# Optimization experiments

Measured on AMD Instinct MI355X. Metric: run time of the kernel, lower is better.

## Reference

```python
import jax, jax.numpy as jnp
import numpy as np

B, C, H, W = 8, 384, 32, 32
HEADS = 12


def _relative_position_index(h, w):
    coords_h = np.arange(h)
    coords_w = np.arange(w)
    coords = np.stack(np.meshgrid(coords_h, coords_w, indexing='ij'))  # [2,h,w]
    flat = coords.reshape(2, -1)  # [2, N]
    rel = flat[:, :, None] - flat[:, None, :]  # [2, N, N]
    rel = rel.transpose(1, 2, 0)  # [N, N, 2]
    rel[:, :, 0] += h - 1
    rel[:, :, 1] += w - 1
    rel[:, :, 0] *= 2 * w - 1
    return rel.sum(-1).astype(np.int32)  # [N, N]


def setup_inputs() -> dict:
    key = jax.random.key(0)
    ks = jax.random.split(key, 6)
    std = 0.02
    x = jax.random.normal(ks[0], (B, C, H, W), dtype=jnp.float32)
    q_w = jax.random.normal(ks[1], (C, C), dtype=jnp.float32) * std
    q_b = jnp.zeros((C,), dtype=jnp.float32)
    kv_w = jax.random.normal(ks[2], (2 * C, C), dtype=jnp.float32) * std
    kv_b = jnp.zeros((2 * C,), dtype=jnp.float32)
    proj_w = jax.random.normal(ks[3], (C, C), dtype=jnp.float32) * std
    proj_b = jnp.zeros((C,), dtype=jnp.float32)
    n_table = (2 * H - 1) * (2 * W - 1)
    rpb_table = jax.random.normal(ks[4], (n_table, HEADS), dtype=jnp.float32) * std
    rel_index = jnp.asarray(_relative_position_index(H, W))  # [N, N] int32
    return {"x": x, "q_w": q_w, "q_b": q_b, "kv_w": kv_w, "kv_b": kv_b,
            "proj_w": proj_w, "proj_b": proj_b, "rpb_table": rpb_table,
            "rel_index": rel_index}


def reference(x, q_w, q_b, kv_w, kv_b, proj_w, proj_b, rpb_table, rel_index):
    b, c, h, w = x.shape
    n = h * w
    heads = rpb_table.shape[-1]
    hd = c // heads
    scale = hd ** (-0.5)

    xf = x.reshape(b, c, n)  # 1x1 conv == per-pixel matmul
    q = jnp.einsum('dc,bcn->bdn', q_w, xf) + q_b[:, None]
    q = q.reshape(b, heads, hd, n).transpose(0, 1, 3, 2)  # [b,h,n,hd]
    kv = jnp.einsum('dc,bcn->bdn', kv_w, xf) + kv_b[:, None]
    kv = kv.reshape(b, 2, heads, hd, n)
    k = kv[:, 0].transpose(0, 1, 3, 2)  # [b,h,n,hd]
    v = kv[:, 1].transpose(0, 1, 3, 2)

    attn = jnp.einsum('bhnd,bhmd->bhnm', q, k) * scale  # [b,h,n,n]
    bias = rpb_table[rel_index.reshape(-1)].reshape(n, n, heads)
    bias = bias.transpose(2, 0, 1)  # [h,n,n]
    attn = jax.nn.softmax(attn + bias[None], axis=-1)

    out = jnp.einsum('bhnm,bhmd->bhnd', attn, v)
    out = out.transpose(0, 1, 3, 2).reshape(b, c, h, w)
    out = jnp.einsum('dc,bchw->bdhw', proj_w, out) + proj_b[None, :, None, None]
    return out
```

## Files before the change

kernel.cpp:

```cpp
#include <hip/hip_runtime.h>
#include <hip/hip_bf16.h>

#define B_  8
#define C_  384
#define N_  1024
#define NH_ 12
#define HD_ 32
#define D3_ 1152

typedef __bf16 bf16x8 __attribute__((ext_vector_type(8)));
typedef __bf16 bf16x2 __attribute__((ext_vector_type(2)));
typedef float  f32x4  __attribute__((ext_vector_type(4)));

typedef const __attribute__((address_space(1))) unsigned int guint;
typedef __attribute__((address_space(3))) unsigned int luint;

__device__ __forceinline__ float b2f(ushort u) {
    return __uint_as_float(((unsigned int)u) << 16);
}
__device__ __forceinline__ ushort f2b(float f) {
    unsigned int i = __float_as_uint(f);
    unsigned int r = i + 0x7fffu + ((i >> 16) & 1u);
    return (ushort)(r >> 16);
}
__device__ __forceinline__ unsigned pk2(float a, float b) {
#if __has_builtin(__builtin_amdgcn_cvt_pk_bf16_f32)
    bf16x2 t = __builtin_amdgcn_cvt_pk_bf16_f32(a, b);
    return __builtin_bit_cast(unsigned, t);
#else
    return (unsigned)f2b(a) | ((unsigned)f2b(b) << 16);
#endif
}

#if __has_builtin(__builtin_amdgcn_exp2f)
#define EXP2 __builtin_amdgcn_exp2f
#else
#define EXP2 exp2f
#endif

__device__ __forceinline__ void gl2lds16(const void* g, void* l) {
    __builtin_amdgcn_global_load_lds((guint*)g, (luint*)l, 16, 0, 0);
}

#define C1_ 0.25505654204433796f
#define C2_ 1.4426950408889634f
#define TS_ 3972

__global__ __launch_bounds__(256) void setup(
    const float* __restrict__ x, const float* __restrict__ q_w,
    const float* __restrict__ kv_w, const float* __restrict__ proj_w,
    const float* __restrict__ q_b, const float* __restrict__ kv_b,
    const float* __restrict__ tab,
    ushort* __restrict__ xT, float* __restrict__ tabT,
    ushort* __restrict__ Wall, ushort* __restrict__ PW,
    float* __restrict__ ballf)
{
    __shared__ ushort T[64 * 72];
    const int bx = blockIdx.x, tid = threadIdx.x;

    if (bx < 768) {
        int t = bx;
        int nx = t & 15, cy = (t >> 4) % 6, b = t / 96;
        int n0 = nx * 64, c0 = cy * 64;
        {
            int i = tid >> 2;
            int ns = (tid & 3) * 16;
            const float* src = x + ((size_t)b * C_ + c0 + i) * N_ + n0 + ns;
            #pragma unroll
            for (int k4 = 0; k4 < 4; ++k4) {
                float4 f = *(const float4*)(src + k4 * 4);
                T[(ns + k4 * 4 + 0) * 72 + i] = f2b(f.x);
                T[(ns + k4 * 4 + 1) * 72 + i] = f2b(f.y);
                T[(ns + k4 * 4 + 2) * 72 + i] = f2b(f.z);
                T[(ns + k4 * 4 + 3) * 72 + i] = f2b(f.w);
            }
        }
        __syncthreads();
        {
            int j = tid >> 2;
            int cs = (tid & 3) * 16;
            ushort* dst = xT + ((size_t)b * N_ + n0 + j) * C_ + c0 + cs;
            *(uint4*)dst       = *(const uint4*)&T[j * 72 + cs];
            *(uint4*)(dst + 8) = *(const uint4*)&T[j * 72 + cs + 8];
        }
    } else if (bx < 1346) {
        const int NW4 = 110592, NP4 = 36864, NB4 = 288;
        int t = (bx - 768) * 256 + tid;
        if (t < NW4) {
            int e = t * 4;
            float4 f = (e < 147456) ? *(const float4*)(q_w + e)
                                    : *(const float4*)(kv_w + e - 147456);
            union { uint2 u; ushort s[4]; } o;
            o.u.x = pk2(f.x, f.y); o.u.y = pk2(f.z, f.w);
            *(uint2*)(Wall + e) = o.u;
        } else if (t < NW4 + NP4) {
            int e = (t - NW4) * 4;
            float4 f = *(const float4*)(proj_w + e);
            union { uint2 u; ushort s[4]; } o;
            o.u.x = pk2(f.x, f.y); o.u.y = pk2(f.z, f.w);
            *(uint2*)(PW + e) = o.u;
        } else if (t < NW4 + NP4 + NB4) {
            int e = (t - NW4 - NP4) * 4;
            float4 f = (e < 384) ? *(const float4*)(q_b + e)
                                 : *(const float4*)(kv_b + e - 384);
            *(float4*)(ballf + e) = f;
        }
    } else {
        int h = bx - 1346;
        for (int i = tid; i < 3969; i += 256)
            tabT[h * TS_ + i] = tab[(size_t)(3968 - i) * NH_ + h] * C2_;
        if (tid < 3) tabT[h * TS_ + 3969 + tid] = 0.0f;
    }
}

__global__ __launch_bounds__(256) void qkv_gemm5(
    const ushort* __restrict__ xT, const ushort* __restrict__ Wall,
    const float* __restrict__ ballf, ushort* __restrict__ Qt,
    ushort* __restrict__ Kt, ushort* __restrict__ Vtc)
{
    const int b = blockIdx.z, n0 = blockIdx.x * 128, d0 = blockIdx.y * 128;
    __shared__ ushort As[128 * 32];
    __shared__ ushort Bs[128 * 32];
    const int tid = threadIdx.x;
    const int lane = tid & 63, wave = tid >> 6;
    const int quad = lane >> 4, l16 = lane & 15;
    const int wn = (wave & 1) * 64, wd = (wave >> 1) * 64;

    f32x4 acc[4][4] = {};
    const ushort* xb = xT + ((size_t)b * N_ + n0) * C_;
    const ushort* wb = Wall + (size_t)d0 * C_;
    const int rowA = wave * 16 + (lane >> 2);
    const int fstage = ((lane >> 2) ^ (lane >> 4)) & 3;
    const int coff = ((lane & 3) ^ fstage) * 8;
    const int fread = ((l16 & 3) ^ ((l16 >> 2) & 3));
    const bool isV = (d0 >= 768);

    for (int c0 = 0; c0 < C_; c0 += 32) {
        #pragma unroll
        for (int k = 0; k < 2; ++k) {
            gl2lds16(xb + (size_t)(k * 64 + rowA) * C_ + c0 + coff,
                     &As[(size_t)(k * 256 + wave * 64) * 8]);
            gl2lds16(wb + (size_t)(k * 64 + rowA) * C_ + c0 + coff,
                     &Bs[(size_t)(k * 256 + wave * 64) * 8]);
        }
        __syncthreads();
        bf16x8 af[4], bfr[4];
        #pragma unroll
        for (int i = 0; i < 4; ++i)
            af[i] = *(const bf16x8*)&As[(wn + i * 16 + l16) * 32 + (quad ^ fread) * 8];
        #pragma unroll
        for (int j = 0; j < 4; ++j)
            bfr[j] = *(const bf16x8*)&Bs[(wd + j * 16 + l16) * 32 + (quad ^ fread) * 8];
        if (!isV) {
            #pragma unroll
            for (int i = 0; i < 4; ++i)
                #pragma unroll
                for (int j = 0; j < 4; ++j)
                    acc[i][j] = __builtin_amdgcn_mfma_f32_16x16x32_bf16(bfr[i], af[j], acc[i][j], 0, 0, 0);
        } else {
            #pragma unroll
            for (int i = 0; i < 4; ++i)
                #pragma unroll
                for (int j = 0; j < 4; ++j)
                    acc[i][j] = __builtin_amdgcn_mfma_f32_16x16x32_bf16(af[i], bfr[j], acc[i][j], 0, 0, 0);
        }
        __syncthreads();
    }

    if (!isV) {
        ushort* dst = (d0 < 384) ? Qt : Kt;
        const float sc = (d0 < 384) ? C1_ : 1.0f;
        const int reg0 = (d0 < 384) ? 0 : 384;
        #pragma unroll
        for (int i = 0; i < 4; ++i) {
            int dloc = wd + i * 16;
            int dg = d0 - reg0 + dloc;
            int h = dg >> 5;
            int dc = (dg & 31) + quad * 4;
            float4 bvv = *(const float4*)(ballf + d0 + dloc + quad * 4);
            size_t hb = (size_t)(b * NH_ + h) * N_;
            #pragma unroll
            for (int j = 0; j < 4; ++j) {
                int n = n0 + wn + j * 16 + l16;
                uint2 w;
                w.x = pk2((acc[i][j][0] + bvv.x) * sc, (acc[i][j][1] + bvv.y) * sc);
                w.y = pk2((acc[i][j][2] + bvv.z) * sc, (acc[i][j][3] + bvv.w) * sc);
                *(uint2*)(dst + (hb + n) * 32 + dc) = w;
            }
        }
    } else {
        #pragma unroll
        for (int j = 0; j < 4; ++j) {
            int dloc = wd + j * 16 + l16;
            int vd = d0 - 768 + dloc;
            int h = vd >> 5, dc = vd & 31;
            float bv = ballf[d0 + dloc];
            size_t hbase = (size_t)(b * NH_ + h) * 32768 + dc * 32;
            #pragma unroll
            for (int i = 0; i < 4; ++i) {
                int n = n0 + wn + i * 16 + quad * 4;
                size_t cbase = hbase + (size_t)((n >> 5)) * 1024 + (n & 31);
                uint2 w;
                w.x = pk2(acc[i][j][0] + bv, acc[i][j][1] + bv);
                w.y = pk2(acc[i][j][2] + bv, acc[i][j][3] + bv);
                *(uint2*)(Vtc + cbase) = w;
            }
        }
    }
}

__global__ __launch_bounds__(256) void attn9(
    const ushort* __restrict__ Qt, const ushort* __restrict__ Kt,
    const ushort* __restrict__ Vtc, const float* __restrict__ tabT,
    ushort* __restrict__ O)
{
    const int bid = blockIdx.x;
    const int bh96 = bid % 96;
    const int nx = bid / 96;
    const int b = bh96 / 12, h = bh96 % 12;

    __shared__ float tabL[TS_];
    __shared__ ushort Pa[8192];

    const int tid = threadIdx.x;
    const int lane = tid & 63, wave = tid >> 6;
    const int quad = lane >> 4, l16 = lane & 15;
    const int bh = b * NH_ + h;

    {
        const float* th = tabT + h * TS_;
        int i = tid * 4;
        #pragma unroll
        for (int k = 0; k < 4; ++k) {
            if (i < TS_) *(float4*)&tabL[i] = *(const float4*)&th[i];
            i += 1024;
        }
    }
    __syncthreads();

    const int qs0 = nx * 8 + wave * 2;
    const ushort* Kbh = Kt + (size_t)bh * N_ * 32;
    const ushort* Vbh = Vtc + (size_t)bh * 16 * 2048;

    bf16x8 qf[2];
    #pragma unroll
    for (int st = 0; st < 2; ++st) {
        int q = (qs0 + st) * 16 + l16;
        qf[st] = *(const bf16x8*)(Qt + ((size_t)bh * N_ + q) * 32 + quad * 8);
    }
    int ibx0;
    {
        int q = qs0 * 16 + l16;
        ibx0 = (31 - (q >> 5)) * 63 + (31 - (q & 31));
    }

    bf16x8 ones;
    #pragma unroll
    for (int j = 0; j < 8; ++j) ones[j] = (__bf16)1.0f;

    f32x4 oacc[2][2] = {};
    f32x4 lacc[2] = {};

    ushort* PwBase = &Pa[wave * 2048];
    const int pswz = l16 & 0xE;

    for (int mc = 0; mc < 16; ++mc) {
        const ushort* kp = Kbh + mc * 64 * 32;
        bf16x8 k0 = *(const bf16x8*)(kp + (0 * 16 + l16) * 32 + quad * 8);
        bf16x8 k1 = *(const bf16x8*)(kp + (1 * 16 + l16) * 32 + quad * 8);
        bf16x8 k2 = *(const bf16x8*)(kp + (2 * 16 + l16) * 32 + quad * 8);
        bf16x8 k3 = *(const bf16x8*)(kp + (3 * 16 + l16) * 32 + quad * 8);
        const ushort* vp = Vbh + mc * 2048;
        bf16x8 va[2][2];
        #pragma unroll
        for (int kc = 0; kc < 2; ++kc)
            #pragma unroll
            for (int dt = 0; dt < 2; ++dt)
                va[kc][dt] = *(const bf16x8*)(vp + kc * 1024 + (dt * 16 + l16) * 32 + quad * 8);

        const float* Tb = tabL + ibx0 + mc * 126 + quad * 4;
        f32x4 tvm16, tv0, tv16, tv47, tv63, tv79;
        #pragma unroll
        for (int e = 0; e < 4; ++e) {
            tvm16[e] = Tb[e - 16];
            tv0[e]   = Tb[e];
            tv16[e]  = Tb[e + 16];
            tv47[e]  = Tb[e + 47];
            tv63[e]  = Tb[e + 63];
            tv79[e]  = Tb[e + 79];
        }
        f32x4 cbs[2][4] = {{tv0, tv16, tv63, tv79}, {tvm16, tv0, tv47, tv63}};

        #pragma unroll
        for (int st = 0; st < 2; ++st) {
            f32x4 s0 = __builtin_amdgcn_mfma_f32_16x16x32_bf16(k0, qf[st], cbs[st][0], 0, 0, 0);
            f32x4 s1 = __builtin_amdgcn_mfma_f32_16x16x32_bf16(k1, qf[st], cbs[st][1], 0, 0, 0);
            f32x4 s2 = __builtin_amdgcn_mfma_f32_16x16x32_bf16(k2, qf[st], cbs[st][2], 0, 0, 0);
            f32x4 s3 = __builtin_amdgcn_mfma_f32_16x16x32_bf16(k3, qf[st], cbs[st][3], 0, 0, 0);

            ushort* Pw = PwBase + st * 1024;
            f32x4 sv[4] = {s0, s1, s2, s3};
            #pragma unroll
            for (int t = 0; t < 4; ++t) {
                float p0 = EXP2(sv[t][0]);
                float p1 = EXP2(sv[t][1]);
                float p2 = EXP2(sv[t][2]);
                float p3 = EXP2(sv[t][3]);
                uint2 w;
                w.x = pk2(p0, p1);
                w.y = pk2(p2, p3);
                *(uint2*)(Pw + l16 * 64 + (((t * 4 + quad) ^ pswz) * 4)) = w;
            }
            #pragma unroll
            for (int kc = 0; kc < 2; ++kc) {
                bf16x8 pb = *(const bf16x8*)(Pw + l16 * 64 + (((kc * 8 + quad * 2) ^ pswz) * 4));
                lacc[st]    = __builtin_amdgcn_mfma_f32_16x16x32_bf16(ones, pb, lacc[st], 0, 0, 0);
                oacc[st][0] = __builtin_amdgcn_mfma_f32_16x16x32_bf16(va[kc][0], pb, oacc[st][0], 0, 0, 0);
                oacc[st][1] = __builtin_amdgcn_mfma_f32_16x16x32_bf16(va[kc][1], pb, oacc[st][1], 0, 0, 0);
            }
        }
    }

    #pragma unroll
    for (int st = 0; st < 2; ++st) {
        float inv = 1.0f / lacc[st][0];
        int q = (qs0 + st) * 16 + l16;
        ushort* ob = O + ((size_t)(b * N_ + q)) * C_ + h * HD_;
        #pragma unroll
        for (int dt = 0; dt < 2; ++dt) {
            uint2 w;
            w.x = pk2(oacc[st][dt][0] * inv, oacc[st][dt][1] * inv);
            w.y = pk2(oacc[st][dt][2] * inv, oacc[st][dt][3] * inv);
            *(uint2*)(ob + dt * 16 + quad * 4) = w;
        }
    }
}

__global__ __launch_bounds__(256) void proj_gemm3(
    const ushort* __restrict__ O, const ushort* __restrict__ PW,
    const float* __restrict__ pb, float* __restrict__ out)
{
    const int b = blockIdx.z, n0 = blockIdx.x * 128, d0 = blockIdx.y * 128;
    __shared__ ushort As[128 * 32];
    __shared__ ushort Bs[128 * 32];
    const int tid = threadIdx.x;
    const int lane = tid & 63, wave = tid >> 6;
    const int quad = lane >> 4, l16 = lane & 15;
    const int wa = (wave & 1) * 64, wb = (wave >> 1) * 64;

    f32x4 acc[4][4] = {};
    const ushort* ab = PW + (size_t)d0 * C_;
    const ushort* bbp = O + ((size_t)b * N_ + n0) * C_;
    const int rowA = wave * 16 + (lane >> 2);
    const int fstage = ((lane >> 2) ^ (lane >> 4)) & 3;
    const int coff = ((lane & 3) ^ fstage) * 8;
    const int fread = ((l16 & 3) ^ ((l16 >> 2) & 3));

    for (int c0 = 0; c0 < C_; c0 += 32) {
        #pragma unroll
        for (int k = 0; k < 2; ++k) {
            gl2lds16(ab + (size_t)(k * 64 + rowA) * C_ + c0 + coff,
                     &As[(size_t)(k * 256 + wave * 64) * 8]);
            gl2lds16(bbp + (size_t)(k * 64 + rowA) * C_ + c0 + coff,
                     &Bs[(size_t)(k * 256 + wave * 64) * 8]);
        }
        __syncthreads();
        bf16x8 af[4], bfr[4];
        #pragma unroll
        for (int i = 0; i < 4; ++i)
            af[i] = *(const bf16x8*)&As[(wa + i * 16 + l16) * 32 + (quad ^ fread) * 8];
        #pragma unroll
        for (int j = 0; j < 4; ++j)
            bfr[j] = *(const bf16x8*)&Bs[(wb + j * 16 + l16) * 32 + (quad ^ fread) * 8];
        #pragma unroll
        for (int i = 0; i < 4; ++i)
            #pragma unroll
            for (int j = 0; j < 4; ++j)
                acc[i][j] = __builtin_amdgcn_mfma_f32_16x16x32_bf16(af[i], bfr[j], acc[i][j], 0, 0, 0);
        __syncthreads();
    }

    #pragma unroll
    for (int i = 0; i < 4; ++i) {
        #pragma unroll
        for (int r = 0; r < 4; ++r) {
            int d = d0 + wa + i * 16 + quad * 4 + r;
            float bv = pb[d];
            float* op = out + ((size_t)b * C_ + d) * N_ + n0 + wb;
            #pragma unroll
            for (int j = 0; j < 4; ++j)
                op[j * 16 + l16] = acc[i][j][r] + bv;
        }
    }
}

extern "C" void kernel_launch(void* const* d_in, const int* in_sizes, int n_in,
                              void* d_out, int out_size, void* d_ws, size_t ws_size,
                              hipStream_t stream)
{
    const float* x      = (const float*)d_in[0];
    const float* q_w    = (const float*)d_in[1];
    const float* q_b    = (const float*)d_in[2];
    const float* kv_w   = (const float*)d_in[3];
    const float* kv_b   = (const float*)d_in[4];
    const float* proj_w = (const float*)d_in[5];
    const float* proj_b = (const float*)d_in[6];
    const float* rpb    = (const float*)d_in[7];
    float* out = (float*)d_out;

    char* ws = (char*)d_ws;
    ushort* xT    = (ushort*)(ws);
    ushort* Qt    = (ushort*)(ws +  6291456);
    ushort* Kt    = (ushort*)(ws + 12582912);
    ushort* Vtc   = (ushort*)(ws + 18874368);
    ushort* O     = (ushort*)(ws + 25165824);
    float*  tabT  = (float*) (ws + 31457280);
    ushort* Wall  = (ushort*)(ws + 31647936);
    ushort* PW    = (ushort*)(ws + 32532672);
    float*  ballf = (float*) (ws + 32827584);

    setup      <<<dim3(1358), 256, 0, stream>>>(x, q_w, kv_w, proj_w, q_b, kv_b, rpb,
                                                xT, tabT, Wall, PW, ballf);
    qkv_gemm5  <<<dim3(8, 9, B_), 256, 0, stream>>>(xT, Wall, ballf, Qt, Kt, Vtc);
    attn9      <<<dim3(768), 256, 0, stream>>>(Qt, Kt, Vtc, tabT, O);
    proj_gemm3 <<<dim3(8, 3, B_), 256, 0, stream>>>(O, PW, proj_b, out);
}
```

Measured before the change: 149.7 us.

## Double-buffer LDS tiles in QKV and projection GEMMs; raise MFMA wave priority in attention

Both GEMM kernels now keep two LDS buffers and issue the direct global-to-LDS loads for the next K-slice before computing on the current one. This drops one barrier per iteration and overlaps load latency with MFMA work. The attention kernel wraps its MFMA blocks in s_setprio so waves that are issuing matrix ops get scheduling priority over waves doing exp and LDS writes. Doubling LDS use per block may lower occupancy. Also, with a single barrier per iteration, the async LDS writes may not be properly waited on before the buffer is read.

```diff
diff --git a/kernel.cpp b/kernel.cpp
--- a/kernel.cpp
+++ b/kernel.cpp
@@ -113,14 +113,14 @@
     }
 }
 
-__global__ __launch_bounds__(256) void qkv_gemm5(
+__global__ __launch_bounds__(256) void qkv_gemm6(
     const ushort* __restrict__ xT, const ushort* __restrict__ Wall,
     const float* __restrict__ ballf, ushort* __restrict__ Qt,
     ushort* __restrict__ Kt, ushort* __restrict__ Vtc)
 {
     const int b = blockIdx.z, n0 = blockIdx.x * 128, d0 = blockIdx.y * 128;
-    __shared__ ushort As[128 * 32];
-    __shared__ ushort Bs[128 * 32];
+    __shared__ ushort As[2][128 * 32];
+    __shared__ ushort Bs[2][128 * 32];
     const int tid = threadIdx.x;
     const int lane = tid & 63, wave = tid >> 6;
     const int quad = lane >> 4, l16 = lane & 15;
@@ -134,23 +134,34 @@
     const int coff = ((lane & 3) ^ fstage) * 8;
     const int fread = ((l16 & 3) ^ ((l16 >> 2) & 3));
     const bool isV = (d0 >= 768);
-
-    for (int c0 = 0; c0 < C_; c0 += 32) {
-        #pragma unroll
-        for (int k = 0; k < 2; ++k) {
-            gl2lds16(xb + (size_t)(k * 64 + rowA) * C_ + c0 + coff,
-                     &As[(size_t)(k * 256 + wave * 64) * 8]);
-            gl2lds16(wb + (size_t)(k * 64 + rowA) * C_ + c0 + coff,
-                     &Bs[(size_t)(k * 256 + wave * 64) * 8]);
-        }
-        __syncthreads();
+    const int lo = wave * 512;
+
+    #pragma unroll
+    for (int k = 0; k < 2; ++k) {
+        gl2lds16(xb + (size_t)(k * 64 + rowA) * C_ + coff, &As[0][k * 2048 + lo]);
+        gl2lds16(wb + (size_t)(k * 64 + rowA) * C_ + coff, &Bs[0][k * 2048 + lo]);
+    }
+    __syncthreads();
+
+    int cur = 0;
+    for (int it = 0; it < 12; ++it) {
+        if (it < 11) {
+            int c0 = (it + 1) * 32;
+            #pragma unroll
+            for (int k = 0; k < 2; ++k) {
+                gl2lds16(xb + (size_t)(k * 64 + rowA) * C_ + c0 + coff,
+                         &As[cur ^ 1][k * 2048 + lo]);
+                gl2lds16(wb + (size_t)(k * 64 + rowA) * C_ + c0 + coff,
+                         &Bs[cur ^ 1][k * 2048 + lo]);
+            }
+        }
         bf16x8 af[4], bfr[4];
         #pragma unroll
         for (int i = 0; i < 4; ++i)
-            af[i] = *(const bf16x8*)&As[(wn + i * 16 + l16) * 32 + (quad ^ fread) * 8];
+            af[i] = *(const bf16x8*)&As[cur][(wn + i * 16 + l16) * 32 + (quad ^ fread) * 8];
         #pragma unroll
         for (int j = 0; j < 4; ++j)
-            bfr[j] = *(const bf16x8*)&Bs[(wd + j * 16 + l16) * 32 + (quad ^ fread) * 8];
+            bfr[j] = *(const bf16x8*)&Bs[cur][(wd + j * 16 + l16) * 32 + (quad ^ fread) * 8];
         if (!isV) {
             #pragma unroll
             for (int i = 0; i < 4; ++i)
@@ -165,6 +176,7 @@
                     acc[i][j] = __builtin_amdgcn_mfma_f32_16x16x32_bf16(af[i], bfr[j], acc[i][j], 0, 0, 0);
         }
         __syncthreads();
+        cur ^= 1;
     }
 
     if (!isV) {
@@ -209,7 +221,7 @@
     }
 }
 
-__global__ __launch_bounds__(256) void attn9(
+__global__ __launch_bounds__(256) void attn10(
     const ushort* __restrict__ Qt, const ushort* __restrict__ Kt,
     const ushort* __restrict__ Vtc, const float* __restrict__ tabT,
     ushort* __restrict__ O)
@@ -293,10 +305,12 @@
 
         #pragma unroll
         for (int st = 0; st < 2; ++st) {
+            __builtin_amdgcn_s_setprio(1);
             f32x4 s0 = __builtin_amdgcn_mfma_f32_16x16x32_bf16(k0, qf[st], cbs[st][0], 0, 0, 0);
             f32x4 s1 = __builtin_amdgcn_mfma_f32_16x16x32_bf16(k1, qf[st], cbs[st][1], 0, 0, 0);
             f32x4 s2 = __builtin_amdgcn_mfma_f32_16x16x32_bf16(k2, qf[st], cbs[st][2], 0, 0, 0);
             f32x4 s3 = __builtin_amdgcn_mfma_f32_16x16x32_bf16(k3, qf[st], cbs[st][3], 0, 0, 0);
+            __builtin_amdgcn_s_setprio(0);
 
             ushort* Pw = PwBase + st * 1024;
             f32x4 sv[4] = {s0, s1, s2, s3};
@@ -311,6 +325,7 @@
                 w.y = pk2(p2, p3);
                 *(uint2*)(Pw + l16 * 64 + (((t * 4 + quad) ^ pswz) * 4)) = w;
             }
+            __builtin_amdgcn_s_setprio(1);
             #pragma unroll
             for (int kc = 0; kc < 2; ++kc) {
                 bf16x8 pb = *(const bf16x8*)(Pw + l16 * 64 + (((kc * 8 + quad * 2) ^ pswz) * 4));
@@ -318,6 +333,7 @@
                 oacc[st][0] = __builtin_amdgcn_mfma_f32_16x16x32_bf16(va[kc][0], pb, oacc[st][0], 0, 0, 0);
                 oacc[st][1] = __builtin_amdgcn_mfma_f32_16x16x32_bf16(va[kc][1], pb, oacc[st][1], 0, 0, 0);
             }
+            __builtin_amdgcn_s_setprio(0);
         }
     }
 
@@ -336,13 +352,13 @@
     }
 }
 
-__global__ __launch_bounds__(256) void proj_gemm3(
+__global__ __launch_bounds__(256) void proj_gemm4(
     const ushort* __restrict__ O, const ushort* __restrict__ PW,
     const float* __restrict__ pb, float* __restrict__ out)
 {
     const int b = blockIdx.z, n0 = blockIdx.x * 128, d0 = blockIdx.y * 128;
-    __shared__ ushort As[128 * 32];
-    __shared__ ushort Bs[128 * 32];
+    __shared__ ushort As[2][128 * 32];
+    __shared__ ushort Bs[2][128 * 32];
     const int tid = threadIdx.x;
     const int lane = tid & 63, wave = tid >> 6;
     const int quad = lane >> 4, l16 = lane & 15;
@@ -355,29 +371,41 @@
     const int fstage = ((lane >> 2) ^ (lane >> 4)) & 3;
     const int coff = ((lane & 3) ^ fstage) * 8;
     const int fread = ((l16 & 3) ^ ((l16 >> 2) & 3));
-
-    for (int c0 = 0; c0 < C_; c0 += 32) {
-        #pragma unroll
-        for (int k = 0; k < 2; ++k) {
-            gl2lds16(ab + (size_t)(k * 64 + rowA) * C_ + c0 + coff,
-                     &As[(size_t)(k * 256 + wave * 64) * 8]);
-            gl2lds16(bbp + (size_t)(k * 64 + rowA) * C_ + c0 + coff,
-                     &Bs[(size_t)(k * 256 + wave * 64) * 8]);
-        }
-        __syncthreads();
+    const int lo = wave * 512;
+
+    #pragma unroll
+    for (int k = 0; k < 2; ++k) {
+        gl2lds16(ab + (size_t)(k * 64 + rowA) * C_ + coff, &As[0][k * 2048 + lo]);
+        gl2lds16(bbp + (size_t)(k * 64 + rowA) * C_ + coff, &Bs[0][k * 2048 + lo]);
+    }
+    __syncthreads();
+
+    int cur = 0;
+    for (int it = 0; it < 12; ++it) {
+        if (it < 11) {
+            int c0 = (it + 1) * 32;
+            #pragma unroll
+            for (int k = 0; k < 2; ++k) {
+                gl2lds16(ab + (size_t)(k * 64 + rowA) * C_ + c0 + coff,
+                         &As[cur ^ 1][k * 2048 + lo]);
+                gl2lds16(bbp + (size_t)(k * 64 + rowA) * C_ + c0 + coff,
+                         &Bs[cur ^ 1][k * 2048 + lo]);
+            }
+        }
         bf16x8 af[4], bfr[4];
         #pragma unroll
         for (int i = 0; i < 4; ++i)
-            af[i] = *(const bf16x8*)&As[(wa + i * 16 + l16) * 32 + (quad ^ fread) * 8];
+            af[i] = *(const bf16x8*)&As[cur][(wa + i * 16 + l16) * 32 + (quad ^ fread) * 8];
         #pragma unroll
         for (int j = 0; j < 4; ++j)
-            bfr[j] = *(const bf16x8*)&Bs[(wb + j * 16 + l16) * 32 + (quad ^ fread) * 8];
+            bfr[j] = *(const bf16x8*)&Bs[cur][(wb + j * 16 + l16) * 32 + (quad ^ fread) * 8];
         #pragma unroll
         for (int i = 0; i < 4; ++i)
             #pragma unroll
             for (int j = 0; j < 4; ++j)
                 acc[i][j] = __builtin_amdgcn_mfma_f32_16x16x32_bf16(af[i], bfr[j], acc[i][j], 0, 0, 0);
         __syncthreads();
+        cur ^= 1;
     }
 
     #pragma unroll
@@ -421,7 +449,7 @@
 
     setup      <<<dim3(1358), 256, 0, stream>>>(x, q_w, kv_w, proj_w, q_b, kv_b, rpb,
                                                 xT, tabT, Wall, PW, ballf);
-    qkv_gemm5  <<<dim3(8, 9, B_), 256, 0, stream>>>(xT, Wall, ballf, Qt, Kt, Vtc);
-    attn9      <<<dim3(768), 256, 0, stream>>>(Qt, Kt, Vtc, tabT, O);
-    proj_gemm3 <<<dim3(8, 3, B_), 256, 0, stream>>>(O, PW, proj_b, out);
-}
+    qkv_gemm6  <<<dim3(8, 9, B_), 256, 0, stream>>>(xT, Wall, ballf, Qt, Kt, Vtc);
+    attn10     <<<dim3(768), 256, 0, stream>>>(Qt, Kt, Vtc, tabT, O);
+    proj_gemm4 <<<dim3(8, 3, B_), 256, 0, stream>>>(O, PW, proj_b, out);
+}
```

After: 149.4 us. Within noise of the previous version (-0.2%).
